# Kernel optimization log

Measured on AMD Instinct MI355X. Metric: run time of the kernel, lower is better.

The kernel has to match this reference:

```python
import jax, jax.numpy as jnp
import numpy as np

# Module hyperparameters (from init_kwargs)
HID = 2048          # hidden_dim
LAT = 512           # kv_latent_dim
H = 16              # num_heads
D = HID // H        # head_dim = 128
FORGET_P = 0.1      # forget_prob
WIN = 128           # window_size
SINK = 16           # persistent_tokens
B, S = 2, 2048
NEG = -1e9


def setup_inputs() -> dict:
    key = jax.random.key(0)
    ks = jax.random.split(key, 8)
    scale = 0.02
    x = jax.random.normal(ks[0], (B, S, HID), dtype=jnp.float32)
    W_q = jax.random.normal(ks[1], (HID, HID), dtype=jnp.float32) * scale
    W_dkv = jax.random.normal(ks[2], (HID, LAT), dtype=jnp.float32) * scale
    W_uk = jax.random.normal(ks[3], (LAT, HID), dtype=jnp.float32) * scale
    W_uv = jax.random.normal(ks[4], (LAT, HID), dtype=jnp.float32) * scale
    W_o = jax.random.normal(ks[5], (HID, HID), dtype=jnp.float32) * scale
    # Bernoulli(forget_prob) per-key forget mask (1 = forget this token)
    forget_mask = jax.random.bernoulli(ks[6], FORGET_P, (B, S)).astype(jnp.int32)
    return {"x": x, "W_q": W_q, "W_dkv": W_dkv, "W_uk": W_uk,
            "W_uv": W_uv, "W_o": W_o, "forget_mask": forget_mask, "top_k": 64}


def reference(x, W_q, W_dkv, W_uk, W_uv, W_o, forget_mask, top_k):
    Bx, Sx, _ = x.shape
    # Queries; keys/values via shared compressed KV latent (MLA-style)
    q = (x @ W_q).reshape(Bx, Sx, H, D)
    c = x @ W_dkv                                   # [B, S, LAT]
    k = (c @ W_uk).reshape(Bx, Sx, H, D)
    v = (c @ W_uv).reshape(Bx, Sx, H, D)

    scores = jnp.einsum('bqhd,bkhd->bhqk', q, k) / np.float32(np.sqrt(D))

    qi = jnp.arange(Sx)[:, None]
    ki = jnp.arange(Sx)[None, :]
    causal = ki <= qi
    local = ki >= qi - (WIN - 1)
    sink = ki < SINK                  # persistent sink tokens always visible
    allow = causal & (local | sink)   # [S, S]

    # Forgetting: drop non-sink, non-self keys flagged by the forget mask
    forget = (forget_mask[:, None, None, :] == 1) \
             & (ki >= SINK)[None, None] & (ki != qi)[None, None]   # [B,1,S,S]
    keep = allow[None, None] & ~forget

    s = jnp.where(keep, scores, jnp.asarray(NEG, scores.dtype))
    # Top-k selection per query: keep only the k largest scores
    kth = jax.lax.top_k(s, top_k)[0][..., -1:]
    s = jnp.where(s >= kth, s, jnp.asarray(NEG, s.dtype))

    attn = jax.nn.softmax(s, axis=-1)
    out = jnp.einsum('bhqk,bkhd->bqhd', attn, v).reshape(Bx, Sx, HID)
    return out @ W_o
```

## Files before the change

kernel.cpp:

```cpp
#include <hip/hip_runtime.h>
#include <hip/hip_bf16.h>

typedef unsigned short u16;
typedef unsigned int u32;
typedef unsigned long long u64;
typedef __bf16 bf16x8 __attribute__((ext_vector_type(8)));
typedef float f32x4 __attribute__((ext_vector_type(4)));
typedef u16 u16x4 __attribute__((ext_vector_type(4)));
typedef u16 u16x8 __attribute__((ext_vector_type(8)));

static constexpr int BB = 2, SS = 2048, HIDC = 2048, LATC = 512, NH = 16, HD = 128;
static constexpr int MROWS = BB * SS;
static constexpr float NEGV = -1e9f;

__device__ __forceinline__ u16 f2bf(float f) {
  __hip_bfloat16 h = __float2bfloat16(f);
  return __builtin_bit_cast(u16, h);
}
__device__ __forceinline__ float bf2f(u16 u) {
  return __uint_as_float(((u32)u) << 16);
}
__device__ __forceinline__ void load_lds16(const void* g, void* l) {
  __builtin_amdgcn_global_load_lds(
      (const __attribute__((address_space(1))) void*)g,
      (__attribute__((address_space(3))) void*)l, 16, 0, 0);
}

template <int MODE>
__global__ __launch_bounds__(256, 2) void gemm_bt(
    const u16* __restrict__ A, const u16* __restrict__ Bt,
    float* __restrict__ C, u16* __restrict__ Cb, int M, int N, int K) {
  __shared__ u16 As[128 * 64];
  __shared__ u16 Bs[128 * 64];
  const int tid = threadIdx.x;
  const int lane = tid & 63;
  const int wv = tid >> 6;
  const int wr = wv >> 1, wc = wv & 1;
  const int m0 = blockIdx.x * 128, n0 = blockIdx.y * 128;

  f32x4 acc[4][4];
#pragma unroll
  for (int i = 0; i < 4; ++i)
#pragma unroll
    for (int j = 0; j < 4; ++j) acc[i][j] = (f32x4){0.f, 0.f, 0.f, 0.f};

  int srow[4], sgc[4];
#pragma unroll
  for (int j = 0; j < 4; ++j) {
    int e = j * 2048 + tid * 8;
    int row = e >> 6;
    int slot = (e >> 3) & 7;
    srow[j] = row;
    sgc[j] = (slot ^ (row & 7)) * 8;
  }

  for (int k0 = 0; k0 < K; k0 += 64) {
    __syncthreads();
#pragma unroll
    for (int j = 0; j < 4; ++j) {
      const u16* ga = A + (size_t)(m0 + srow[j]) * K + k0 + sgc[j];
      const u16* gb = Bt + (size_t)(n0 + srow[j]) * K + k0 + sgc[j];
      load_lds16(ga, &As[j * 2048 + wv * 512]);
      load_lds16(gb, &Bs[j * 2048 + wv * 512]);
    }
    asm volatile("s_waitcnt vmcnt(0)" ::: "memory");
    __syncthreads();

#pragma unroll
    for (int kk = 0; kk < 2; ++kk) {
      bf16x8 afr[4], bfr[4];
      const int kg = kk * 4 + (lane >> 4);
#pragma unroll
      for (int i = 0; i < 4; ++i) {
        int ar = wr * 64 + i * 16 + (lane & 15);
        afr[i] = *(const bf16x8*)&As[ar * 64 + ((kg ^ (ar & 7)) << 3)];
        int br = wc * 64 + i * 16 + (lane & 15);
        bfr[i] = *(const bf16x8*)&Bs[br * 64 + ((kg ^ (br & 7)) << 3)];
      }
#pragma unroll
      for (int mi = 0; mi < 4; ++mi)
#pragma unroll
        for (int ni = 0; ni < 4; ++ni)
          acc[mi][ni] = __builtin_amdgcn_mfma_f32_16x16x32_bf16(
              afr[mi], bfr[ni], acc[mi][ni], 0, 0, 0);
    }
  }

#pragma unroll
  for (int mi = 0; mi < 4; ++mi) {
#pragma unroll
    for (int ni = 0; ni < 4; ++ni) {
      const int row = m0 + wr * 64 + mi * 16 + (lane >> 4) * 4;
      const int col = n0 + wc * 64 + ni * 16 + (lane & 15);
#pragma unroll
      for (int r = 0; r < 4; ++r) {
        size_t off = (size_t)(row + r) * N + col;
        if constexpr (MODE == 0) C[off] = acc[mi][ni][r];
        if constexpr (MODE == 2) Cb[off] = f2bf(acc[mi][ni][r]);
      }
    }
  }
}

template <int TN, int MODE>
__global__ __launch_bounds__(256, 2) void gemm_split_bt(
    const u16* __restrict__ Ah, const u16* __restrict__ Al,
    const u16* __restrict__ Bth, const u16* __restrict__ Btl,
    float* __restrict__ C, u16* __restrict__ Cb, int M, int N, int K) {
  constexpr int NI = TN / 32;
  __shared__ u16 Ash[128 * 64];
  __shared__ u16 Asl[128 * 64];
  __shared__ u16 Bsh[TN * 64];
  __shared__ u16 Bsl[TN * 64];
  const int tid = threadIdx.x;
  const int lane = tid & 63;
  const int wv = tid >> 6;
  const int wr = wv >> 1, wc = wv & 1;
  const int l15 = lane & 15, lhi = lane >> 4;
  const int m0 = blockIdx.x * 128, n0 = blockIdx.y * TN;

  f32x4 acc[4][NI];
#pragma unroll
  for (int i = 0; i < 4; ++i)
#pragma unroll
    for (int j = 0; j < NI; ++j) acc[i][j] = (f32x4){0.f, 0.f, 0.f, 0.f};

  int srow[4], sgc[4];
#pragma unroll
  for (int j = 0; j < 4; ++j) {
    int e = j * 2048 + tid * 8;
    int row = e >> 6;
    int slot = (e >> 3) & 7;
    srow[j] = row;
    sgc[j] = (slot ^ (row & 7)) * 8;
  }

  for (int k0 = 0; k0 < K; k0 += 64) {
    __syncthreads();
#pragma unroll
    for (int j = 0; j < 4; ++j) {
      const size_t ao = (size_t)(m0 + srow[j]) * K + k0 + sgc[j];
      load_lds16(Ah + ao, &Ash[j * 2048 + wv * 512]);
      load_lds16(Al + ao, &Asl[j * 2048 + wv * 512]);
    }
#pragma unroll
    for (int j = 0; j < NI; ++j) {
      const size_t bo = (size_t)(n0 + srow[j]) * K + k0 + sgc[j];
      load_lds16(Bth + bo, &Bsh[j * 2048 + wv * 512]);
      load_lds16(Btl + bo, &Bsl[j * 2048 + wv * 512]);
    }
    asm volatile("s_waitcnt vmcnt(0)" ::: "memory");
    __syncthreads();

#pragma unroll
    for (int kk = 0; kk < 2; ++kk) {
      const int kg = kk * 4 + lhi;
      bf16x8 afh[4], afl[4], bfh[NI], bfl[NI];
#pragma unroll
      for (int i = 0; i < 4; ++i) {
        const int ar = wr * 64 + i * 16 + l15;
        const int off = ar * 64 + ((kg ^ (ar & 7)) << 3);
        afh[i] = *(const bf16x8*)&Ash[off];
        afl[i] = *(const bf16x8*)&Asl[off];
      }
#pragma unroll
      for (int i = 0; i < NI; ++i) {
        const int br = wc * (TN / 2) + i * 16 + l15;
        const int off = br * 64 + ((kg ^ (br & 7)) << 3);
        bfh[i] = *(const bf16x8*)&Bsh[off];
        bfl[i] = *(const bf16x8*)&Bsl[off];
      }
#pragma unroll
      for (int mi = 0; mi < 4; ++mi)
#pragma unroll
        for (int ni = 0; ni < NI; ++ni) {
          acc[mi][ni] = __builtin_amdgcn_mfma_f32_16x16x32_bf16(
              afh[mi], bfh[ni], acc[mi][ni], 0, 0, 0);
          acc[mi][ni] = __builtin_amdgcn_mfma_f32_16x16x32_bf16(
              afh[mi], bfl[ni], acc[mi][ni], 0, 0, 0);
          acc[mi][ni] = __builtin_amdgcn_mfma_f32_16x16x32_bf16(
              afl[mi], bfh[ni], acc[mi][ni], 0, 0, 0);
        }
    }
  }

#pragma unroll
  for (int mi = 0; mi < 4; ++mi) {
#pragma unroll
    for (int ni = 0; ni < NI; ++ni) {
      const int row = m0 + wr * 64 + mi * 16 + lhi * 4;
      const int col = n0 + wc * (TN / 2) + ni * 16 + l15;
#pragma unroll
      for (int r = 0; r < 4; ++r) {
        size_t off = (size_t)(row + r) * N + col;
        if constexpr (MODE == 0) C[off] = acc[mi][ni][r];
        if constexpr (MODE == 2) Cb[off] = f2bf(acc[mi][ni][r]);
      }
    }
  }
}

__global__ __launch_bounds__(1024) void transpose_split(
    const float* __restrict__ W, u16* __restrict__ Th, u16* __restrict__ Tl,
    int K, int N) {
  __shared__ float t[32][33];
  const int tx = threadIdx.x, ty = threadIdx.y;
  t[ty][tx] = W[(size_t)(blockIdx.y * 32 + ty) * N + blockIdx.x * 32 + tx];
  __syncthreads();
  const float v = t[tx][ty];
  const u16 hi = f2bf(v);
  const u16 lo = f2bf(v - bf2f(hi));
  const size_t o = (size_t)(blockIdx.x * 32 + ty) * K + blockIdx.y * 32 + tx;
  Th[o] = hi;
  Tl[o] = lo;
}

__global__ __launch_bounds__(1024) void transpose_one(
    const float* __restrict__ W, u16* __restrict__ T, int K, int N) {
  __shared__ float t[32][33];
  const int tx = threadIdx.x, ty = threadIdx.y;
  t[ty][tx] = W[(size_t)(blockIdx.y * 32 + ty) * N + blockIdx.x * 32 + tx];
  __syncthreads();
  const size_t o = (size_t)(blockIdx.x * 32 + ty) * K + blockIdx.y * 32 + tx;
  T[o] = f2bf(t[tx][ty]);
}

__global__ void split_ew(const float* __restrict__ in, u16* __restrict__ hi,
                         u16* __restrict__ lo, int n) {
  const size_t i = ((size_t)blockIdx.x * blockDim.x + threadIdx.x) * 4;
  if (i >= (size_t)n) return;
  f32x4 v = *(const f32x4*)(in + i);
  u16x4 h, l;
#pragma unroll
  for (int e = 0; e < 4; ++e) {
    float f = v[e];
    u16 hh = f2bf(f);
    h[e] = hh;
    l[e] = f2bf(f - bf2f(hh));
  }
  *(u16x4*)(hi + i) = h;
  *(u16x4*)(lo + i) = l;
}

__device__ __forceinline__ u32 fmap(float f) {
  u32 b = __float_as_uint(f);
  return (b & 0x80000000u) ? ~b : (b | 0x80000000u);
}
__device__ __forceinline__ float unfmap(u32 u) {
  return (u & 0x80000000u) ? __uint_as_float(u ^ 0x80000000u)
                           : __uint_as_float(~u);
}

__global__ __launch_bounds__(512, 4) void attn_v3(
    const float* __restrict__ qf, const float* __restrict__ kf,
    const u16* __restrict__ vt, const int* __restrict__ forget,
    const int* __restrict__ topk, u16* __restrict__ ab) {
  __shared__ u16 KP[2 * 64 * 128];
  __shared__ float St[64 * 68];
  __shared__ int fm[256];

  u16* const Kh = KP;
  u16* const Kl = KP + 64 * 128;
  u16* const Pb = KP;
  u16* const Vts = (u16*)St;

  const float scale = 0.08838834764831845f;
  const int tid = threadIdx.x, lane = tid & 63, wv = tid >> 6;
  const int q0 = blockIdx.x * 64;
  const int h = blockIdx.y, b = blockIdx.z;
  const int mt = wv >> 1, nh = wv & 1;
  const int l15 = lane & 15, lhi = lane >> 4;

  const int nt = (q0 >= 256) ? 4 : (q0 / 64 + 1);
  const int KTOP = topk[0];

  auto kbase = [&](int t) {
    return (q0 >= 256) ? (t == 0 ? 0 : q0 + t * 64 - 192) : t * 64;
  };
  auto stage_vt = [&](int T) {
    const int kbt = kbase(T);
#pragma unroll
    for (int p = 0; p < 2; ++p) {
      const int c = p * 512 + tid;
      const int d = c >> 3, sl = c & 7;
      const u16* src = vt + ((size_t)(b * HIDC + h * HD + d)) * SS + kbt +
                       ((sl ^ (d & 7)) << 3);
      load_lds16(src, Vts + (p * 512 + wv * 64) * 8);
    }
  };

  if (tid < 256) {
    const int t = tid >> 6;
    fm[tid] = (t < nt) ? forget[b * SS + kbase(t) + (tid & 63)] : 0;
  }

  u16x8 ah[4], al[4];
  {
    const size_t qrow = (size_t)(b * SS + q0 + mt * 16 + l15) * HIDC + h * HD;
#pragma unroll
    for (int kt = 0; kt < 4; ++kt)
#pragma unroll
      for (int hf = 0; hf < 2; ++hf) {
        f32x4 v = *(const f32x4*)(qf + qrow + kt * 32 + lhi * 8 + hf * 4);
#pragma unroll
        for (int e = 0; e < 4; ++e) {
          const u16 hi = f2bf(v[e]);
          ah[kt][hf * 4 + e] = hi;
          al[kt][hf * 4 + e] = f2bf(v[e] - bf2f(hi));
        }
      }
  }

  u32 uu[8][4];
#pragma unroll
  for (int i = 0; i < 8; ++i)
#pragma unroll
    for (int j = 0; j < 4; ++j) uu[i][j] = 0u;

#pragma unroll
  for (int t = 0; t < 4; ++t) {
    if (t < nt) {
      const int kbt = kbase(t);
      __syncthreads();
      for (int idx = tid; idx < 64 * 32; idx += 512) {
        const int row = idx >> 5, c4 = idx & 31;
        f32x4 v = *(const f32x4*)(kf + (size_t)(b * SS + kbt + row) * HIDC +
                                  h * HD + c4 * 4);
        u16x4 hh, ll;
#pragma unroll
        for (int e = 0; e < 4; ++e) {
          const u16 hi = f2bf(v[e]);
          hh[e] = hi;
          ll[e] = f2bf(v[e] - bf2f(hi));
        }
        const int off = row * 128 + (((c4 >> 1) ^ (row & 7)) << 3) + (c4 & 1) * 4;
        *(u16x4*)(Kh + off) = hh;
        *(u16x4*)(Kl + off) = ll;
      }
      __syncthreads();

      f32x4 acc0 = (f32x4){0.f, 0.f, 0.f, 0.f};
      f32x4 acc1 = (f32x4){0.f, 0.f, 0.f, 0.f};
#pragma unroll
      for (int kt = 0; kt < 4; ++kt) {
        const int kg = kt * 4 + lhi;
#pragma unroll
        for (int ni = 0; ni < 2; ++ni) {
          const int key = nh * 32 + ni * 16 + l15;
          const int off = key * 128 + ((kg ^ (key & 7)) << 3);
          bf16x8 bh = *(const bf16x8*)(Kh + off);
          bf16x8 bl = *(const bf16x8*)(Kl + off);
          f32x4 a = ni ? acc1 : acc0;
          a = __builtin_amdgcn_mfma_f32_16x16x32_bf16(
              __builtin_bit_cast(bf16x8, ah[kt]), bh, a, 0, 0, 0);
          a = __builtin_amdgcn_mfma_f32_16x16x32_bf16(
              __builtin_bit_cast(bf16x8, ah[kt]), bl, a, 0, 0, 0);
          a = __builtin_amdgcn_mfma_f32_16x16x32_bf16(
              __builtin_bit_cast(bf16x8, al[kt]), bh, a, 0, 0, 0);
          if (ni) acc1 = a; else acc0 = a;
        }
      }
#pragma unroll
      for (int ni = 0; ni < 2; ++ni)
#pragma unroll
        for (int r = 0; r < 4; ++r)
          St[(mt * 16 + lhi * 4 + r) * 68 + nh * 32 + ni * 16 + l15] =
              (ni ? acc1 : acc0)[r] * scale;
      __syncthreads();

#pragma unroll
      for (int i = 0; i < 8; ++i) {
        const int r = wv * 8 + i, qi = q0 + r;
        const int key = kbt + lane;
        const bool valid =
            key <= qi && (key >= qi - 127 || key < 16) &&
            !(fm[t * 64 + lane] && key >= 16 && key != qi);
        const float sv = valid ? St[r * 68 + lane] : NEGV;
        uu[i][t] = fmap(sv);
      }
    }
  }
  __syncthreads();

  stage_vt(0);

  u32 tl[8], th[8];
#pragma unroll
  for (int i = 0; i < 8; ++i) { tl[i] = 0u; th[i] = 0xFFFFFFFFu; }
  for (int it = 0; it < 32; ++it) {
#pragma unroll
    for (int i = 0; i < 8; ++i) {
      const u32 mid = tl[i] + ((th[i] - tl[i]) >> 1) + 1u;
      const int cnt = __popcll(__ballot(uu[i][0] >= mid)) +
                      __popcll(__ballot(uu[i][1] >= mid)) +
                      __popcll(__ballot(uu[i][2] >= mid)) +
                      __popcll(__ballot(uu[i][3] >= mid));
      const bool ge = cnt >= KTOP;
      tl[i] = ge ? mid : tl[i];
      th[i] = ge ? th[i] : mid - 1u;
    }
  }

  float mrow[8];
#pragma unroll
  for (int i = 0; i < 8; ++i) {
    float mm = NEGV;
#pragma unroll
    for (int j = 0; j < 4; ++j) {
      const float s = unfmap(uu[i][j]);
      mm = (uu[i][j] >= tl[i]) ? fmaxf(mm, s) : mm;
    }
    mrow[i] = mm;
  }
#pragma unroll
  for (int off = 32; off > 0; off >>= 1)
#pragma unroll
    for (int i = 0; i < 8; ++i) mrow[i] = fmaxf(mrow[i], __shfl_xor(mrow[i], off));

  float zrow[8];
#pragma unroll
  for (int i = 0; i < 8; ++i) {
    float zz = 0.f;
#pragma unroll
    for (int j = 0; j < 4; ++j) {
      const float s = unfmap(uu[i][j]);
      zz += (uu[i][j] >= tl[i]) ? __expf(s - mrow[i]) : 0.f;
    }
    zrow[i] = zz;
  }
#pragma unroll
  for (int off = 32; off > 0; off >>= 1)
#pragma unroll
    for (int i = 0; i < 8; ++i) zrow[i] += __shfl_xor(zrow[i], off);

#pragma unroll
  for (int i = 0; i < 8; ++i) {
    const int r = wv * 8 + i;
    const float rz = 1.f / zrow[i];
#pragma unroll
    for (int j = 0; j < 4; ++j) {
      const float s = unfmap(uu[i][j]);
      const float p =
          (uu[i][j] >= tl[i]) ? __expf(s - mrow[i]) * rz : 0.f;
      const int c = lane + 64 * j;
      const int sl = c >> 3;
      Pb[r * 256 + ((sl ^ (r & 7)) << 3) + (c & 7)] = f2bf(p);
    }
  }

  asm volatile("s_waitcnt vmcnt(0)" ::: "memory");
  __syncthreads();

  f32x4 pacc[4];
#pragma unroll
  for (int t2 = 0; t2 < 4; ++t2) pacc[t2] = (f32x4){0.f, 0.f, 0.f, 0.f};

#pragma unroll
  for (int t = 0; t < 4; ++t) {
    if (t < nt) {
#pragma unroll
      for (int ks = 0; ks < 2; ++ks) {
        const int arow = mt * 16 + l15;
        const int aslot = t * 8 + ks * 4 + lhi;
        const bf16x8 af =
            *(const bf16x8*)(Pb + arow * 256 + ((aslot ^ (arow & 7)) << 3));
#pragma unroll
        for (int t2 = 0; t2 < 4; ++t2) {
          const int drow = nh * 64 + t2 * 16 + l15;
          const int dslot = ks * 4 + lhi;
          const bf16x8 bf_ =
              *(const bf16x8*)(Vts + drow * 64 + ((dslot ^ (drow & 7)) << 3));
          pacc[t2] = __builtin_amdgcn_mfma_f32_16x16x32_bf16(af, bf_, pacc[t2],
                                                             0, 0, 0);
        }
      }
      if (t + 1 < nt) {
        __syncthreads();
        stage_vt(t + 1);
        asm volatile("s_waitcnt vmcnt(0)" ::: "memory");
        __syncthreads();
      }
    }
  }

#pragma unroll
  for (int t2 = 0; t2 < 4; ++t2)
#pragma unroll
    for (int r = 0; r < 4; ++r) {
      const int row = q0 + mt * 16 + lhi * 4 + r;
      const int col = h * HD + nh * 64 + t2 * 16 + l15;
      ab[(size_t)(b * SS + row) * HIDC + col] = f2bf(pacc[t2][r]);
    }
}

extern "C" void kernel_launch(void* const* d_in, const int* in_sizes, int n_in,
                              void* d_out, int out_size, void* d_ws, size_t ws_size,
                              hipStream_t stream) {
  const float* x = (const float*)d_in[0];
  const float* W_q = (const float*)d_in[1];
  const float* W_dkv = (const float*)d_in[2];
  const float* W_uk = (const float*)d_in[3];
  const float* W_uv = (const float*)d_in[4];
  const float* W_o = (const float*)d_in[5];
  const int* forget = (const int*)d_in[6];
  const int* topk = (const int*)d_in[7];
  float* out = (float*)d_out;

  char* p = (char*)d_ws;
  auto take = [&](size_t n) {
    char* r = p;
    p += (n + 255) & ~(size_t)255;
    return r;
  };

  u16* xb_hi = (u16*)take((size_t)MROWS * HIDC * 2);
  u16* xb_lo = (u16*)take((size_t)MROWS * HIDC * 2);
  u16* Wqh = (u16*)take((size_t)HIDC * HIDC * 2);
  u16* Wql = (u16*)take((size_t)HIDC * HIDC * 2);
  u16* Wdh = (u16*)take((size_t)LATC * HIDC * 2);
  u16* Wdl = (u16*)take((size_t)LATC * HIDC * 2);
  u16* Wukh = (u16*)take((size_t)HIDC * LATC * 2);
  u16* Wukl = (u16*)take((size_t)HIDC * LATC * 2);
  u16* Wuvt = (u16*)take((size_t)HIDC * LATC * 2);
  u16* Wot = (u16*)take((size_t)HIDC * HIDC * 2);
  float* qf = (float*)take((size_t)MROWS * HIDC * 4);
  float* cf = (float*)take((size_t)MROWS * LATC * 4);
  u16* cbh = (u16*)take((size_t)MROWS * LATC * 2);
  u16* cbl = (u16*)take((size_t)MROWS * LATC * 2);
  u16* vt = (u16*)take((size_t)BB * HIDC * SS * 2);
  float* kf = (float*)xb_hi;
  u16* ab = Wqh;

  const dim3 tb(32, 32);
  split_ew<<<dim3((MROWS * HIDC / 4) / 256), dim3(256), 0, stream>>>(
      x, xb_hi, xb_lo, MROWS * HIDC);
  transpose_split<<<dim3(HIDC / 32, HIDC / 32), tb, 0, stream>>>(W_q, Wqh, Wql, HIDC, HIDC);
  transpose_split<<<dim3(LATC / 32, HIDC / 32), tb, 0, stream>>>(W_dkv, Wdh, Wdl, HIDC, LATC);
  transpose_split<<<dim3(HIDC / 32, LATC / 32), tb, 0, stream>>>(W_uk, Wukh, Wukl, LATC, HIDC);
  transpose_one<<<dim3(HIDC / 32, LATC / 32), tb, 0, stream>>>(W_uv, Wuvt, LATC, HIDC);
  transpose_one<<<dim3(HIDC / 32, HIDC / 32), tb, 0, stream>>>(W_o, Wot, HIDC, HIDC);

  gemm_split_bt<128, 0><<<dim3(MROWS / 128, HIDC / 128), 256, 0, stream>>>(
      xb_hi, xb_lo, Wqh, Wql, qf, nullptr, MROWS, HIDC, HIDC);
  gemm_split_bt<64, 0><<<dim3(MROWS / 128, LATC / 64), 256, 0, stream>>>(
      xb_hi, xb_lo, Wdh, Wdl, cf, nullptr, MROWS, LATC, HIDC);
  split_ew<<<dim3((MROWS * LATC / 4) / 256), dim3(256), 0, stream>>>(
      cf, cbh, cbl, MROWS * LATC);
  gemm_split_bt<128, 0><<<dim3(MROWS / 128, HIDC / 128), 256, 0, stream>>>(
      cbh, cbl, Wukh, Wukl, kf, nullptr, MROWS, HIDC, LATC);
  const dim3 gv(HIDC / 128, SS / 128);
  gemm_bt<2><<<gv, 256, 0, stream>>>(Wuvt, cbh, nullptr, vt, HIDC, SS, LATC);
  gemm_bt<2><<<gv, 256, 0, stream>>>(Wuvt, cbh + (size_t)SS * LATC, nullptr,
                                     vt + (size_t)HIDC * SS, HIDC, SS, LATC);
  attn_v3<<<dim3(SS / 64, NH, BB), dim3(512), 0, stream>>>(
      qf, kf, vt, forget, topk, ab);
  gemm_bt<0><<<dim3(MROWS / 128, HIDC / 128), 256, 0, stream>>>(
      ab, Wot, out, nullptr, MROWS, HIDC, HIDC);
}
```

Measured before the change: 358.1 us.

## Emit split bf16 hi/lo from GEMM epilogues and restructure attention to 4 waves

The projection GEMMs now write split bf16 hi/lo outputs directly, which removes the fp32 q/c/k buffers and the separate split_ew pass on the latent. The attention kernel drops from 8 to 4 waves per block, each wave owning 16 query rows across all keys and head dims. It stages pre-split K tiles into LDS with async global_load_lds, prefetching the next tile while the current one is scored. The intent is to cut global traffic and per-element conversion work, at the cost of doubling per-wave register state (uu[16][4], pacc[8]), which may limit occupancy.

```diff
diff --git a/kernel.cpp b/kernel.cpp
--- a/kernel.cpp
+++ b/kernel.cpp
@@ -106,7 +106,8 @@
 __global__ __launch_bounds__(256, 2) void gemm_split_bt(
     const u16* __restrict__ Ah, const u16* __restrict__ Al,
     const u16* __restrict__ Bth, const u16* __restrict__ Btl,
-    float* __restrict__ C, u16* __restrict__ Cb, int M, int N, int K) {
+    float* __restrict__ C, u16* __restrict__ Ch, u16* __restrict__ Cl,
+    int M, int N, int K) {
   constexpr int NI = TN / 32;
   __shared__ u16 Ash[128 * 64];
   __shared__ u16 Asl[128 * 64];
@@ -192,9 +193,14 @@
       const int col = n0 + wc * (TN / 2) + ni * 16 + l15;
 #pragma unroll
       for (int r = 0; r < 4; ++r) {
-        size_t off = (size_t)(row + r) * N + col;
-        if constexpr (MODE == 0) C[off] = acc[mi][ni][r];
-        if constexpr (MODE == 2) Cb[off] = f2bf(acc[mi][ni][r]);
+        const size_t off = (size_t)(row + r) * N + col;
+        const float v = acc[mi][ni][r];
+        if constexpr (MODE == 0) C[off] = v;
+        if constexpr (MODE == 3) {
+          const u16 hh = f2bf(v);
+          Ch[off] = hh;
+          Cl[off] = f2bf(v - bf2f(hh));
+        }
       }
     }
   }
@@ -251,14 +257,14 @@
                            : __uint_as_float(~u);
 }
 
-__global__ __launch_bounds__(512, 4) void attn_v3(
-    const float* __restrict__ qf, const float* __restrict__ kf,
+__global__ __launch_bounds__(256, 3) void attn_v4(
+    const u16* __restrict__ qbh, const u16* __restrict__ qbl,
+    const u16* __restrict__ khi, const u16* __restrict__ klo,
     const u16* __restrict__ vt, const int* __restrict__ forget,
     const int* __restrict__ topk, u16* __restrict__ ab) {
   __shared__ u16 KP[2 * 64 * 128];
   __shared__ float St[64 * 68];
   __shared__ int fm[256];
-
   u16* const Kh = KP;
   u16* const Kl = KP + 64 * 128;
   u16* const Pb = KP;
@@ -268,115 +274,98 @@
   const int tid = threadIdx.x, lane = tid & 63, wv = tid >> 6;
   const int q0 = blockIdx.x * 64;
   const int h = blockIdx.y, b = blockIdx.z;
-  const int mt = wv >> 1, nh = wv & 1;
   const int l15 = lane & 15, lhi = lane >> 4;
-
   const int nt = (q0 >= 256) ? 4 : (q0 / 64 + 1);
   const int KTOP = topk[0];
 
   auto kbase = [&](int t) {
     return (q0 >= 256) ? (t == 0 ? 0 : q0 + t * 64 - 192) : t * 64;
   };
-  auto stage_vt = [&](int T) {
-    const int kbt = kbase(T);
-#pragma unroll
-    for (int p = 0; p < 2; ++p) {
-      const int c = p * 512 + tid;
+  auto stage_k = [&](int t) {
+    const int kbt = kbase(t);
+#pragma unroll
+    for (int p = 0; p < 4; ++p) {
+      const int c = p * 256 + tid;
+      const int row = c >> 4, sl = c & 15;
+      const size_t src = (size_t)(b * SS + kbt + row) * HIDC + h * HD +
+                         ((sl ^ (row & 7)) << 3);
+      load_lds16(khi + src, Kh + (p * 256 + wv * 64) * 8);
+      load_lds16(klo + src, Kl + (p * 256 + wv * 64) * 8);
+    }
+  };
+  auto stage_vt = [&](int t) {
+    const int kbt = kbase(t);
+#pragma unroll
+    for (int p = 0; p < 4; ++p) {
+      const int c = p * 256 + tid;
       const int d = c >> 3, sl = c & 7;
       const u16* src = vt + ((size_t)(b * HIDC + h * HD + d)) * SS + kbt +
                        ((sl ^ (d & 7)) << 3);
-      load_lds16(src, Vts + (p * 512 + wv * 64) * 8);
+      load_lds16(src, Vts + (p * 256 + wv * 64) * 8);
     }
   };
 
-  if (tid < 256) {
-    const int t = tid >> 6;
-    fm[tid] = (t < nt) ? forget[b * SS + kbase(t) + (tid & 63)] : 0;
-  }
+  fm[tid] = ((tid >> 6) < nt) ? forget[b * SS + kbase(tid >> 6) + (tid & 63)] : 0;
 
   u16x8 ah[4], al[4];
-  {
-    const size_t qrow = (size_t)(b * SS + q0 + mt * 16 + l15) * HIDC + h * HD;
-#pragma unroll
-    for (int kt = 0; kt < 4; ++kt)
-#pragma unroll
-      for (int hf = 0; hf < 2; ++hf) {
-        f32x4 v = *(const f32x4*)(qf + qrow + kt * 32 + lhi * 8 + hf * 4);
-#pragma unroll
-        for (int e = 0; e < 4; ++e) {
-          const u16 hi = f2bf(v[e]);
-          ah[kt][hf * 4 + e] = hi;
-          al[kt][hf * 4 + e] = f2bf(v[e] - bf2f(hi));
-        }
-      }
-  }
-
-  u32 uu[8][4];
-#pragma unroll
-  for (int i = 0; i < 8; ++i)
+  const size_t qrow = (size_t)(b * SS + q0 + wv * 16 + l15) * HIDC + h * HD;
+#pragma unroll
+  for (int kt = 0; kt < 4; ++kt) {
+    ah[kt] = *(const u16x8*)(qbh + qrow + kt * 32 + lhi * 8);
+    al[kt] = *(const u16x8*)(qbl + qrow + kt * 32 + lhi * 8);
+  }
+
+  u32 uu[16][4];
+#pragma unroll
+  for (int i = 0; i < 16; ++i)
 #pragma unroll
     for (int j = 0; j < 4; ++j) uu[i][j] = 0u;
 
+  stage_k(0);
 #pragma unroll
   for (int t = 0; t < 4; ++t) {
     if (t < nt) {
-      const int kbt = kbase(t);
+      asm volatile("s_waitcnt vmcnt(0)" ::: "memory");
       __syncthreads();
-      for (int idx = tid; idx < 64 * 32; idx += 512) {
-        const int row = idx >> 5, c4 = idx & 31;
-        f32x4 v = *(const f32x4*)(kf + (size_t)(b * SS + kbt + row) * HIDC +
-                                  h * HD + c4 * 4);
-        u16x4 hh, ll;
-#pragma unroll
-        for (int e = 0; e < 4; ++e) {
-          const u16 hi = f2bf(v[e]);
-          hh[e] = hi;
-          ll[e] = f2bf(v[e] - bf2f(hi));
-        }
-        const int off = row * 128 + (((c4 >> 1) ^ (row & 7)) << 3) + (c4 & 1) * 4;
-        *(u16x4*)(Kh + off) = hh;
-        *(u16x4*)(Kl + off) = ll;
-      }
-      __syncthreads();
-
-      f32x4 acc0 = (f32x4){0.f, 0.f, 0.f, 0.f};
-      f32x4 acc1 = (f32x4){0.f, 0.f, 0.f, 0.f};
+
+      f32x4 acc[4];
+#pragma unroll
+      for (int ni = 0; ni < 4; ++ni) acc[ni] = (f32x4){0.f, 0.f, 0.f, 0.f};
 #pragma unroll
       for (int kt = 0; kt < 4; ++kt) {
         const int kg = kt * 4 + lhi;
 #pragma unroll
-        for (int ni = 0; ni < 2; ++ni) {
-          const int key = nh * 32 + ni * 16 + l15;
+        for (int ni = 0; ni < 4; ++ni) {
+          const int key = ni * 16 + l15;
           const int off = key * 128 + ((kg ^ (key & 7)) << 3);
-          bf16x8 bh = *(const bf16x8*)(Kh + off);
-          bf16x8 bl = *(const bf16x8*)(Kl + off);
-          f32x4 a = ni ? acc1 : acc0;
-          a = __builtin_amdgcn_mfma_f32_16x16x32_bf16(
-              __builtin_bit_cast(bf16x8, ah[kt]), bh, a, 0, 0, 0);
-          a = __builtin_amdgcn_mfma_f32_16x16x32_bf16(
-              __builtin_bit_cast(bf16x8, ah[kt]), bl, a, 0, 0, 0);
-          a = __builtin_amdgcn_mfma_f32_16x16x32_bf16(
-              __builtin_bit_cast(bf16x8, al[kt]), bh, a, 0, 0, 0);
-          if (ni) acc1 = a; else acc0 = a;
+          const bf16x8 bh = *(const bf16x8*)(Kh + off);
+          const bf16x8 bl = *(const bf16x8*)(Kl + off);
+          acc[ni] = __builtin_amdgcn_mfma_f32_16x16x32_bf16(
+              __builtin_bit_cast(bf16x8, ah[kt]), bh, acc[ni], 0, 0, 0);
+          acc[ni] = __builtin_amdgcn_mfma_f32_16x16x32_bf16(
+              __builtin_bit_cast(bf16x8, ah[kt]), bl, acc[ni], 0, 0, 0);
+          acc[ni] = __builtin_amdgcn_mfma_f32_16x16x32_bf16(
+              __builtin_bit_cast(bf16x8, al[kt]), bh, acc[ni], 0, 0, 0);
         }
       }
 #pragma unroll
-      for (int ni = 0; ni < 2; ++ni)
+      for (int ni = 0; ni < 4; ++ni)
 #pragma unroll
         for (int r = 0; r < 4; ++r)
-          St[(mt * 16 + lhi * 4 + r) * 68 + nh * 32 + ni * 16 + l15] =
-              (ni ? acc1 : acc0)[r] * scale;
+          St[(wv * 16 + lhi * 4 + r) * 68 + ni * 16 + l15] = acc[ni][r] * scale;
       __syncthreads();
 
-#pragma unroll
-      for (int i = 0; i < 8; ++i) {
-        const int r = wv * 8 + i, qi = q0 + r;
+      if (t + 1 < nt) stage_k(t + 1);
+
+      const int kbt = kbase(t);
+#pragma unroll
+      for (int i = 0; i < 16; ++i) {
+        const int qi = q0 + wv * 16 + i;
         const int key = kbt + lane;
         const bool valid =
             key <= qi && (key >= qi - 127 || key < 16) &&
             !(fm[t * 64 + lane] && key >= 16 && key != qi);
-        const float sv = valid ? St[r * 68 + lane] : NEGV;
-        uu[i][t] = fmap(sv);
+        uu[i][t] = fmap(valid ? St[(wv * 16 + i) * 68 + lane] : NEGV);
       }
     }
   }
@@ -384,12 +373,12 @@
 
   stage_vt(0);
 
-  u32 tl[8], th[8];
-#pragma unroll
-  for (int i = 0; i < 8; ++i) { tl[i] = 0u; th[i] = 0xFFFFFFFFu; }
+  u32 tl[16], th[16];
+#pragma unroll
+  for (int i = 0; i < 16; ++i) { tl[i] = 0u; th[i] = 0xFFFFFFFFu; }
   for (int it = 0; it < 32; ++it) {
 #pragma unroll
-    for (int i = 0; i < 8; ++i) {
+    for (int i = 0; i < 16; ++i) {
       const u32 mid = tl[i] + ((th[i] - tl[i]) >> 1) + 1u;
       const int cnt = __popcll(__ballot(uu[i][0] >= mid)) +
                       __popcll(__ballot(uu[i][1] >= mid)) +
@@ -401,72 +390,53 @@
     }
   }
 
-  float mrow[8];
-#pragma unroll
-  for (int i = 0; i < 8; ++i) {
-    float mm = NEGV;
+#pragma unroll
+  for (int i = 0; i < 16; ++i) {
+    const int r = wv * 16 + i;
+    float sv[4], m = NEGV;
 #pragma unroll
     for (int j = 0; j < 4; ++j) {
-      const float s = unfmap(uu[i][j]);
-      mm = (uu[i][j] >= tl[i]) ? fmaxf(mm, s) : mm;
-    }
-    mrow[i] = mm;
-  }
-#pragma unroll
-  for (int off = 32; off > 0; off >>= 1)
-#pragma unroll
-    for (int i = 0; i < 8; ++i) mrow[i] = fmaxf(mrow[i], __shfl_xor(mrow[i], off));
-
-  float zrow[8];
-#pragma unroll
-  for (int i = 0; i < 8; ++i) {
-    float zz = 0.f;
+      sv[j] = unfmap(uu[i][j]);
+      m = (uu[i][j] >= tl[i]) ? fmaxf(m, sv[j]) : m;
+    }
+#pragma unroll
+    for (int off = 32; off > 0; off >>= 1) m = fmaxf(m, __shfl_xor(m, off));
+    float e[4], z = 0.f;
 #pragma unroll
     for (int j = 0; j < 4; ++j) {
-      const float s = unfmap(uu[i][j]);
-      zz += (uu[i][j] >= tl[i]) ? __expf(s - mrow[i]) : 0.f;
-    }
-    zrow[i] = zz;
-  }
-#pragma unroll
-  for (int off = 32; off > 0; off >>= 1)
-#pragma unroll
-    for (int i = 0; i < 8; ++i) zrow[i] += __shfl_xor(zrow[i], off);
-
-#pragma unroll
-  for (int i = 0; i < 8; ++i) {
-    const int r = wv * 8 + i;
-    const float rz = 1.f / zrow[i];
+      e[j] = (uu[i][j] >= tl[i]) ? __expf(sv[j] - m) : 0.f;
+      z += e[j];
+    }
+#pragma unroll
+    for (int off = 32; off > 0; off >>= 1) z += __shfl_xor(z, off);
+    const float rz = 1.f / z;
 #pragma unroll
     for (int j = 0; j < 4; ++j) {
-      const float s = unfmap(uu[i][j]);
-      const float p =
-          (uu[i][j] >= tl[i]) ? __expf(s - mrow[i]) * rz : 0.f;
       const int c = lane + 64 * j;
       const int sl = c >> 3;
-      Pb[r * 256 + ((sl ^ (r & 7)) << 3) + (c & 7)] = f2bf(p);
+      Pb[r * 256 + ((sl ^ (r & 7)) << 3) + (c & 7)] = f2bf(e[j] * rz);
     }
   }
 
   asm volatile("s_waitcnt vmcnt(0)" ::: "memory");
   __syncthreads();
 
-  f32x4 pacc[4];
-#pragma unroll
-  for (int t2 = 0; t2 < 4; ++t2) pacc[t2] = (f32x4){0.f, 0.f, 0.f, 0.f};
+  f32x4 pacc[8];
+#pragma unroll
+  for (int t2 = 0; t2 < 8; ++t2) pacc[t2] = (f32x4){0.f, 0.f, 0.f, 0.f};
 
 #pragma unroll
   for (int t = 0; t < 4; ++t) {
     if (t < nt) {
 #pragma unroll
       for (int ks = 0; ks < 2; ++ks) {
-        const int arow = mt * 16 + l15;
+        const int arow = wv * 16 + l15;
         const int aslot = t * 8 + ks * 4 + lhi;
         const bf16x8 af =
             *(const bf16x8*)(Pb + arow * 256 + ((aslot ^ (arow & 7)) << 3));
 #pragma unroll
-        for (int t2 = 0; t2 < 4; ++t2) {
-          const int drow = nh * 64 + t2 * 16 + l15;
+        for (int t2 = 0; t2 < 8; ++t2) {
+          const int drow = t2 * 16 + l15;
           const int dslot = ks * 4 + lhi;
           const bf16x8 bf_ =
               *(const bf16x8*)(Vts + drow * 64 + ((dslot ^ (drow & 7)) << 3));
@@ -484,11 +454,11 @@
   }
 
 #pragma unroll
-  for (int t2 = 0; t2 < 4; ++t2)
+  for (int t2 = 0; t2 < 8; ++t2)
 #pragma unroll
     for (int r = 0; r < 4; ++r) {
-      const int row = q0 + mt * 16 + lhi * 4 + r;
-      const int col = h * HD + nh * 64 + t2 * 16 + l15;
+      const int row = q0 + wv * 16 + lhi * 4 + r;
+      const int col = h * HD + t2 * 16 + l15;
       ab[(size_t)(b * SS + row) * HIDC + col] = f2bf(pacc[t2][r]);
     }
 }
@@ -523,12 +493,13 @@
   u16* Wukl = (u16*)take((size_t)HIDC * LATC * 2);
   u16* Wuvt = (u16*)take((size_t)HIDC * LATC * 2);
   u16* Wot = (u16*)take((size_t)HIDC * HIDC * 2);
-  float* qf = (float*)take((size_t)MROWS * HIDC * 4);
-  float* cf = (float*)take((size_t)MROWS * LATC * 4);
+  u16* qbh = (u16*)take((size_t)MROWS * HIDC * 2);
+  u16* qbl = (u16*)take((size_t)MROWS * HIDC * 2);
   u16* cbh = (u16*)take((size_t)MROWS * LATC * 2);
   u16* cbl = (u16*)take((size_t)MROWS * LATC * 2);
   u16* vt = (u16*)take((size_t)BB * HIDC * SS * 2);
-  float* kf = (float*)xb_hi;
+  u16* khi = xb_hi;
+  u16* klo = xb_lo;
   u16* ab = Wqh;
 
   const dim3 tb(32, 32);
@@ -540,20 +511,18 @@
   transpose_one<<<dim3(HIDC / 32, LATC / 32), tb, 0, stream>>>(W_uv, Wuvt, LATC, HIDC);
   transpose_one<<<dim3(HIDC / 32, HIDC / 32), tb, 0, stream>>>(W_o, Wot, HIDC, HIDC);
 
-  gemm_split_bt<128, 0><<<dim3(MROWS / 128, HIDC / 128), 256, 0, stream>>>(
-      xb_hi, xb_lo, Wqh, Wql, qf, nullptr, MROWS, HIDC, HIDC);
-  gemm_split_bt<64, 0><<<dim3(MROWS / 128, LATC / 64), 256, 0, stream>>>(
-      xb_hi, xb_lo, Wdh, Wdl, cf, nullptr, MROWS, LATC, HIDC);
-  split_ew<<<dim3((MROWS * LATC / 4) / 256), dim3(256), 0, stream>>>(
-      cf, cbh, cbl, MROWS * LATC);
-  gemm_split_bt<128, 0><<<dim3(MROWS / 128, HIDC / 128), 256, 0, stream>>>(
-      cbh, cbl, Wukh, Wukl, kf, nullptr, MROWS, HIDC, LATC);
+  gemm_split_bt<128, 3><<<dim3(MROWS / 128, HIDC / 128), 256, 0, stream>>>(
+      xb_hi, xb_lo, Wqh, Wql, nullptr, qbh, qbl, MROWS, HIDC, HIDC);
+  gemm_split_bt<64, 3><<<dim3(MROWS / 128, LATC / 64), 256, 0, stream>>>(
+      xb_hi, xb_lo, Wdh, Wdl, nullptr, cbh, cbl, MROWS, LATC, HIDC);
+  gemm_split_bt<128, 3><<<dim3(MROWS / 128, HIDC / 128), 256, 0, stream>>>(
+      cbh, cbl, Wukh, Wukl, nullptr, khi, klo, MROWS, HIDC, LATC);
   const dim3 gv(HIDC / 128, SS / 128);
   gemm_bt<2><<<gv, 256, 0, stream>>>(Wuvt, cbh, nullptr, vt, HIDC, SS, LATC);
   gemm_bt<2><<<gv, 256, 0, stream>>>(Wuvt, cbh + (size_t)SS * LATC, nullptr,
                                      vt + (size_t)HIDC * SS, HIDC, SS, LATC);
-  attn_v3<<<dim3(SS / 64, NH, BB), dim3(512), 0, stream>>>(
-      qf, kf, vt, forget, topk, ab);
+  attn_v4<<<dim3(SS / 64, NH, BB), dim3(256), 0, stream>>>(
+      qbh, qbl, khi, klo, vt, forget, topk, ab);
   gemm_bt<0><<<dim3(MROWS / 128, HIDC / 128), 256, 0, stream>>>(
       ab, Wot, out, nullptr, MROWS, HIDC, HIDC);
 }
```

After: 369.7 us. 3.2% more time.
